# Kernel tuning notes

Measured on AMD Instinct MI355X. Metric: run time of the kernel, lower is better.

The kernel has to match this reference:

```python
import jax, jax.numpy as jnp
import numpy as np

D_MODEL = 1024
H = 16
D_K = D_MODEL // H
B = 2
S = 2048


def setup_inputs() -> dict:
    key = jax.random.key(0)
    ks = jax.random.split(key, 13)
    scale = 1.0 / np.sqrt(D_MODEL)
    inp = {
        "Q": jax.random.normal(ks[0], (B, S, D_MODEL), jnp.float32),
        "K": jax.random.normal(ks[1], (B, S, D_MODEL), jnp.float32),
        "V": jax.random.normal(ks[2], (B, S, D_MODEL), jnp.float32),
        "mask": jax.random.randint(ks[3], (B, 1, S, S), 0, 2, jnp.int32),
        "WQ_w": jax.random.normal(ks[4], (D_MODEL, D_MODEL), jnp.float32) * scale,
        "WQ_b": jax.random.normal(ks[5], (D_MODEL,), jnp.float32) * scale,
        "WK_w": jax.random.normal(ks[6], (D_MODEL, D_MODEL), jnp.float32) * scale,
        "WK_b": jax.random.normal(ks[7], (D_MODEL,), jnp.float32) * scale,
        "WV_w": jax.random.normal(ks[8], (D_MODEL, D_MODEL), jnp.float32) * scale,
        "WV_b": jax.random.normal(ks[9], (D_MODEL,), jnp.float32) * scale,
        "WO_w": jax.random.normal(ks[10], (D_MODEL, D_MODEL), jnp.float32) * scale,
        "WO_b": jax.random.normal(ks[11], (D_MODEL,), jnp.float32) * scale,
    }
    return inp


def _split_heads(x):
    # [B,S,D] -> [B,H,S,d_k]
    b, s, _ = x.shape
    return x.reshape(b, s, H, D_K).transpose(0, 2, 1, 3)


def reference(Q, K, V, mask, WQ_w, WQ_b, WK_w, WK_b, WV_w, WV_b, WO_w, WO_b):
    q = _split_heads(Q @ WQ_w.T + WQ_b)
    k = _split_heads(K @ WK_w.T + WK_b)
    v = _split_heads(V @ WV_w.T + WV_b)
    scores = jnp.einsum("bhqd,bhkd->bhqk", q, k) / jnp.sqrt(jnp.float32(D_K))
    # NOTE: original code fills masked positions with 1e-9 (not -inf) -- replicate faithfully
    scores = jnp.where(mask == 0, jnp.float32(1e-9), scores)
    attn = jax.nn.softmax(scores, axis=-1)
    out = jnp.einsum("bhqk,bhkd->bhqd", attn, v)  # [B,H,S,d_k]
    out = out.transpose(0, 2, 1, 3).reshape(Q.shape[0], -1, D_MODEL)
    return out @ WO_w.T + WO_b
```

## Files before the change

### kernel.cpp

```cpp
#include <hip/hip_runtime.h>
#include <stdint.h>

#define D_MODEL 1024
#define NH 16
#define DKK 64
#define SEQ 2048
#define QSCALE 0.18033688011112042f

using half8 = __attribute__((ext_vector_type(8))) _Float16;
using half4 = __attribute__((ext_vector_type(4))) _Float16;
using half2v = __attribute__((ext_vector_type(2))) _Float16;
using fp16x2 = __attribute__((ext_vector_type(2))) __fp16;
using f32x4 = __attribute__((ext_vector_type(4))) float;
using f32x16 = __attribute__((ext_vector_type(16))) float;

__device__ __forceinline__ f32x4 fz4() { f32x4 v = {0.f, 0.f, 0.f, 0.f}; return v; }

__device__ __forceinline__ void gload16(const void* g, void* l) {
    __builtin_amdgcn_global_load_lds(
        (const __attribute__((address_space(1))) unsigned int*)g,
        (__attribute__((address_space(3))) unsigned int*)l, 16, 0, 0);
}

__device__ __forceinline__ half2v pk2(float a, float b) {
    fp16x2 t = __builtin_amdgcn_cvt_pkrtz(a, b);
    return __builtin_bit_cast(half2v, t);
}

__device__ __forceinline__ half4 pk4(float a, float b, float c, float d) {
    half2v lo = pk2(a, b);
    half2v hi = pk2(c, d);
    half4 r; r.x = lo.x; r.y = lo.y; r.z = hi.x; r.w = hi.y;
    return r;
}

__device__ __forceinline__ int xswz(int bid, int n) {
    return (bid & 7) * (n >> 3) + (bid >> 3);
}

__global__ __launch_bounds__(256) void conv_all(const float* __restrict__ wq,
                                                const float* __restrict__ wk,
                                                const float* __restrict__ wv,
                                                const float* __restrict__ wo,
                                                const float* __restrict__ Q,
                                                const float* __restrict__ K,
                                                const float* __restrict__ V,
                                                _Float16* __restrict__ out) {
    int idx = blockIdx.x * 256 + threadIdx.x;
#pragma unroll
    for (int k = 0; k < 8; ++k) {
        int c = idx + k * 524288;
        const float* src;
        int off;
        if (c < 1048576) {
            int w = c >> 18;
            src = (w == 0) ? wq : (w == 1) ? wk : (w == 2) ? wv : wo;
            off = c & 0x3ffff;
        } else {
            int j = (c >> 20) - 1;
            src = (j == 0) ? Q : (j == 1) ? K : V;
            off = c & 0xfffff;
        }
        float4 v = ((const float4*)src)[off];
        ((half4*)out)[c] = pk4(v.x, v.y, v.z, v.w);
    }
}

__global__ __launch_bounds__(256) void pack_mask_k(const int* __restrict__ mask,
                                                   unsigned int* __restrict__ mbits) {
    int wid = threadIdx.x >> 6, lane = threadIdx.x & 63;
    int row = blockIdx.x * 4 + wid;
    const int* mrow = mask + (size_t)row * SEQ;
    unsigned int* orow = mbits + (size_t)row * (SEQ / 32);
    for (int it = 0; it < SEQ / 64; ++it) {
        int v = mrow[it * 64 + lane];
        unsigned long long bal = __ballot(v != 0);
        if (lane == 0)       orow[it * 2]     = (unsigned int)(bal & 0xffffffffull);
        else if (lane == 32) orow[it * 2 + 1] = (unsigned int)(bal >> 32);
    }
}

__device__ __forceinline__ void gemm_body(const _Float16* __restrict__ A,
                                          const _Float16* __restrict__ Wh,
                                          const float* __restrict__ bias,
                                          void* __restrict__ outp, int omode, float scale) {
    __shared__ __align__(16) _Float16 Asm[2][64 * 64];
    __shared__ __align__(16) _Float16 Bsm[2][128 * 64];
    const int tid = threadIdx.x;
    const int wg = xswz(blockIdx.x, 512);
    const int bm = wg >> 3, bn = wg & 7;
    const int wid = tid >> 6, lane = tid & 63;
    const int li = lane & 15, g = lane >> 4;
    const int wm = wid >> 1, wn = wid & 1;

    const int brow = wid * 32 + (lane >> 3);
    const char* bsrc = (const char*)(Wh + (size_t)(bn * 128 + brow) * D_MODEL)
                       + (((lane & 7) ^ (brow & 7)) * 16);
    const int bdst = wid * 32 * 128;
    const int arow = wid * 16 + (lane >> 3);
    const char* asrc = (const char*)(A + (size_t)(bm * 64 + arow) * D_MODEL)
                       + (((lane & 7) ^ (arow & 7)) * 16);
    const int adst = wid * 16 * 128;

    f32x4 acc[2][4];
#pragma unroll
    for (int i = 0; i < 2; ++i)
#pragma unroll
        for (int j = 0; j < 4; ++j) acc[i][j] = fz4();

    const int o0 = ((g << 4))      ^ ((li & 7) << 4);
    const int o1 = (64 + (g << 4)) ^ ((li & 7) << 4);
    const int abase = wm * 4096 + li * 128;
    const int bbase = wn * 8192 + li * 128;

    auto stage = [&](int it, int buf) {
        const char* bs = bsrc + it * 128;
        char* bd = (char*)&Bsm[buf][0] + bdst;
        gload16(bs,             bd);
        gload16(bs +  8 * 2048, bd + 1024);
        gload16(bs + 16 * 2048, bd + 2048);
        gload16(bs + 24 * 2048, bd + 3072);
        const char* as = asrc + it * 128;
        char* ad = (char*)&Asm[buf][0] + adst;
        gload16(as,            ad);
        gload16(as + 8 * 2048, ad + 1024);
    };

    stage(0, 0);
    __syncthreads();

    for (int it = 0; it < 16; ++it) {
        const int cur = it & 1;
        if (it + 1 < 16) stage(it + 1, cur ^ 1);
        const char* ab = (const char*)&Asm[cur][0];
        const char* bb = (const char*)&Bsm[cur][0];
#pragma unroll
        for (int s = 0; s < 2; ++s) {
            const int oS = s ? o1 : o0;
            half8 af0 = *(const half8*)(ab + abase + 0    + oS);
            half8 af1 = *(const half8*)(ab + abase + 2048 + oS);
            half8 bf[4];
#pragma unroll
            for (int nt = 0; nt < 4; ++nt)
                bf[nt] = *(const half8*)(bb + bbase + nt * 2048 + oS);
#pragma unroll
            for (int nt = 0; nt < 4; ++nt) {
                acc[0][nt] = __builtin_amdgcn_mfma_f32_16x16x32_f16(af0, bf[nt], acc[0][nt], 0, 0, 0);
                acc[1][nt] = __builtin_amdgcn_mfma_f32_16x16x32_f16(af1, bf[nt], acc[1][nt], 0, 0, 0);
            }
        }
        __syncthreads();
    }

#pragma unroll
    for (int nt = 0; nt < 4; ++nt) {
        int n = bn * 128 + wn * 64 + nt * 16 + li;
        float bv = bias[n];
#pragma unroll
        for (int mt = 0; mt < 2; ++mt) {
            if (omode == 1) {
                int s0 = bm * 64 + wm * 32 + mt * 16 + g * 4;
                int b = (bm * 64) >> 11;
                int h = n >> 6, d = n & 63;
                half4 hv = pk4(acc[mt][nt][0] + bv, acc[mt][nt][1] + bv,
                               acc[mt][nt][2] + bv, acc[mt][nt][3] + bv);
                *(half4*)((_Float16*)outp +
                          ((((size_t)(b * NH + h)) * DKK + d) * SEQ + (s0 & (SEQ - 1)))) = hv;
            } else {
#pragma unroll
                for (int r = 0; r < 4; ++r) {
                    int m = bm * 64 + wm * 32 + mt * 16 + g * 4 + r;
                    float val = (acc[mt][nt][r] + bv) * scale;
                    if (omode == 2) {
                        ((float*)outp)[(size_t)m * D_MODEL + n] = val;
                    } else {
                        int b = m >> 11, s = m & (SEQ - 1);
                        int h = n >> 6, d = n & 63;
                        ((_Float16*)outp)[(((size_t)(b * NH + h)) * SEQ + s) * DKK + d] =
                            (_Float16)val;
                    }
                }
            }
        }
    }
}

struct QkvArgs {
    const float *b0, *b1, *b2;
    _Float16 *o0, *o1, *o2;
};

__global__ __launch_bounds__(256) void gemm_qkv(const _Float16* __restrict__ Ah,
                                                const _Float16* __restrict__ cw,
                                                QkvArgs ga) {
    const int z = blockIdx.y;
    const _Float16* A  = Ah + (size_t)z * (D_MODEL * 4096);
    const float* bi = (z == 0) ? ga.b0 : (z == 1) ? ga.b1 : ga.b2;
    _Float16*    o  = (z == 0) ? ga.o0 : (z == 1) ? ga.o1 : ga.o2;
    gemm_body(A, cw + (size_t)z * D_MODEL * D_MODEL, bi, o,
              (z == 2) ? 1 : 0, (z == 0) ? QSCALE : 1.0f);
}

__global__ __launch_bounds__(256) void gemm_out(const _Float16* __restrict__ A,
                                                const _Float16* __restrict__ cw,
                                                const float* __restrict__ bias,
                                                float* __restrict__ out) {
    gemm_body(A, cw, bias, out, 2, 1.0f);
}

__global__ __launch_bounds__(256, 4) void attn_fwd(const _Float16* __restrict__ q,
                                                   const _Float16* __restrict__ kk,
                                                   const _Float16* __restrict__ vt,
                                                   const unsigned int* __restrict__ mb,
                                                   _Float16* __restrict__ aout) {
    __shared__ __align__(16) char smem[32768];
    const int wg = xswz(blockIdx.x, 1024);
    const int qblk = wg & 31, bh = wg >> 5;
    const int b = bh >> 4, h = bh & 15;
    const int tid = threadIdx.x, wid = tid >> 6, lane = tid & 63;
    const int l31 = lane & 31, hi = lane >> 5;
    const int qh = wid & 1, kh = wid >> 1;
    const _Float16* qp = q  + (size_t)bh * SEQ * DKK;
    const _Float16* kp = kk + (size_t)bh * SEQ * DKK;
    const _Float16* vp = vt + (size_t)bh * DKK * SEQ;
    const int qrow = qblk * 64 + qh * 32 + l31;

    half8 qf[4];
#pragma unroll
    for (int s = 0; s < 4; ++s)
        qf[s] = *(const half8*)(qp + (size_t)qrow * DKK + s * 16 + hi * 8);

    const int srow = wid * 16 + (lane >> 3);
    const int sswz = ((lane & 7) ^ (srow & 7)) * 16;
    const char* ksrc = (const char*)(kp + (size_t)srow * DKK) + sswz;
    const char* vsrc = (const char*)(vp + (size_t)srow * SEQ) + sswz;
    const int sdst = wid * 2048;

    auto stage = [&](int it, int buf) {
        const char* ks = ksrc + (size_t)it * 8192;
        const char* vs = vsrc + (size_t)it * 128;
        char* kd = smem + buf * 8192 + sdst;
        char* vd = smem + 16384 + buf * 8192 + sdst;
        gload16(ks,                       kd);
        gload16(ks + 8 * 128,             kd + 1024);
        gload16(vs,                       vd);
        gload16(vs + 8 * (size_t)SEQ * 2, vd + 1024);
    };

    f32x16 O0, O1;
#pragma unroll
    for (int j = 0; j < 16; ++j) { O0[j] = 0.f; O1[j] = 0.f; }
    float lsum = 0.f;

    const unsigned int* mrow = mb + (size_t)(b * SEQ + qrow) * (SEQ / 32);

    const int krow = kh * 32 + l31;
    const int kbase = krow * 128;
    const int krx = (krow & 7);
    const int v0row = l31;
    const int v1row = 32 + l31;

    stage(0, 0);
    __syncthreads();

    for (int it = 0; it < SEQ / 64; ++it) {
        const int cur = it & 1;
        if (it + 1 < SEQ / 64) stage(it + 1, cur ^ 1);
        const unsigned mw = mrow[it * 2 + kh] >> (hi * 4);

        f32x16 st;
#pragma unroll
        for (int j = 0; j < 16; ++j) st[j] = 0.f;
        const char* kb_ = smem + cur * 8192;
        __builtin_amdgcn_s_setprio(1);
#pragma unroll
        for (int s = 0; s < 4; ++s) {
            const int c = s * 2 + hi;
            half8 kf = *(const half8*)(kb_ + kbase + ((c ^ krx) << 4));
            st = __builtin_amdgcn_mfma_f32_32x32x16_f16(kf, qf[s], st, 0, 0, 0);
        }
        __builtin_amdgcn_s_setprio(0);

        unsigned w[8];
#pragma unroll
        for (int rq = 0; rq < 4; ++rq) {
            float e0 = __builtin_amdgcn_exp2f(st[rq * 4 + 0]);
            float e1 = __builtin_amdgcn_exp2f(st[rq * 4 + 1]);
            float e2 = __builtin_amdgcn_exp2f(st[rq * 4 + 2]);
            float e3 = __builtin_amdgcn_exp2f(st[rq * 4 + 3]);
            float p0 = ((mw >> (8 * rq + 0)) & 1u) ? e0 : 1.0f;
            float p1 = ((mw >> (8 * rq + 1)) & 1u) ? e1 : 1.0f;
            float p2 = ((mw >> (8 * rq + 2)) & 1u) ? e2 : 1.0f;
            float p3 = ((mw >> (8 * rq + 3)) & 1u) ? e3 : 1.0f;
            lsum += (p0 + p1) + (p2 + p3);
            w[2 * rq]     = __builtin_bit_cast(unsigned, pk2(p0, p1));
            w[2 * rq + 1] = __builtin_bit_cast(unsigned, pk2(p2, p3));
        }

        half8 pfrag[2];
#pragma unroll
        for (int s2 = 0; s2 < 2; ++s2) {
            unsigned a0 = w[s2 * 4 + 0], a1 = w[s2 * 4 + 1];
            unsigned a2 = w[s2 * 4 + 2], a3 = w[s2 * 4 + 3];
            unsigned t0 = (unsigned)__shfl_xor((int)(hi ? a0 : a2), 32);
            unsigned t1 = (unsigned)__shfl_xor((int)(hi ? a1 : a3), 32);
            uint4 f;
            f.x = hi ? t0 : a0;
            f.y = hi ? t1 : a1;
            f.z = hi ? a2 : t0;
            f.w = hi ? a3 : t1;
            pfrag[s2] = __builtin_bit_cast(half8, f);
        }

        const char* vb_ = smem + 16384 + cur * 8192;
        __builtin_amdgcn_s_setprio(1);
#pragma unroll
        for (int s2 = 0; s2 < 2; ++s2) {
            const int c = kh * 4 + s2 * 2 + hi;
            half8 vf0 = *(const half8*)(vb_ + v0row * 128 + ((c ^ (v0row & 7)) << 4));
            half8 vf1 = *(const half8*)(vb_ + v1row * 128 + ((c ^ (v1row & 7)) << 4));
            O0 = __builtin_amdgcn_mfma_f32_32x32x16_f16(vf0, pfrag[s2], O0, 0, 0, 0);
            O1 = __builtin_amdgcn_mfma_f32_32x32x16_f16(vf1, pfrag[s2], O1, 0, 0, 0);
        }
        __builtin_amdgcn_s_setprio(0);
        __syncthreads();
    }

    lsum += __shfl_xor(lsum, 32);

    const int SSTR = 36;
    float* scr = (float*)smem;
    float* lscr = (float*)(smem + 2 * 64 * SSTR * 4);
    if (kh == 1) {
        float* dst = scr + (size_t)qh * (64 * SSTR) + lane * SSTR;
#pragma unroll
        for (int j = 0; j < 4; ++j) {
            *(f32x4*)(dst + j * 4)      = *((f32x4*)&O0 + j);
            *(f32x4*)(dst + 16 + j * 4) = *((f32x4*)&O1 + j);
        }
        if (hi == 0) lscr[qh * 32 + l31] = lsum;
    }
    __syncthreads();
    if (kh == 0) {
        const float* src = scr + (size_t)qh * (64 * SSTR) + lane * SSTR;
#pragma unroll
        for (int j = 0; j < 16; ++j) { O0[j] += src[j]; O1[j] += src[16 + j]; }
        float inv = 1.0f / (lsum + lscr[qh * 32 + l31]);
        _Float16* orow = aout + ((size_t)(b * SEQ + qrow)) * D_MODEL + h * DKK + hi * 4;
#pragma unroll
        for (int rq = 0; rq < 4; ++rq) {
            *(half4*)(orow + 8 * rq) =
                pk4(O0[rq * 4 + 0] * inv, O0[rq * 4 + 1] * inv,
                    O0[rq * 4 + 2] * inv, O0[rq * 4 + 3] * inv);
            *(half4*)(orow + 32 + 8 * rq) =
                pk4(O1[rq * 4 + 0] * inv, O1[rq * 4 + 1] * inv,
                    O1[rq * 4 + 2] * inv, O1[rq * 4 + 3] * inv);
        }
    }
}

extern "C" void kernel_launch(void* const* d_in, const int* in_sizes, int n_in,
                              void* d_out, int out_size, void* d_ws, size_t ws_size,
                              hipStream_t stream) {
    const float* Q    = (const float*)d_in[0];
    const float* Kin  = (const float*)d_in[1];
    const float* Vin  = (const float*)d_in[2];
    const int*   mask = (const int*)d_in[3];
    const float* WQw = (const float*)d_in[4];
    const float* WQb = (const float*)d_in[5];
    const float* WKw = (const float*)d_in[6];
    const float* WKb = (const float*)d_in[7];
    const float* WVw = (const float*)d_in[8];
    const float* WVb = (const float*)d_in[9];
    const float* WOw = (const float*)d_in[10];
    const float* WOb = (const float*)d_in[11];

    char* w = (char*)d_ws;
    const size_t MB = 1ull << 20;
    _Float16* cw  = (_Float16*)(w);
    _Float16* Ah  = (_Float16*)(w + 8 * MB);
    _Float16* ab  = (_Float16*)(w + 8 * MB);
    _Float16* qb  = (_Float16*)(w + 32 * MB);
    _Float16* kbf = (_Float16*)(w + 40 * MB);
    _Float16* vtb = (_Float16*)(w + 48 * MB);
    unsigned int* mbits = (unsigned int*)(w + 56 * MB);

    conv_all<<<dim3(2048), dim3(256), 0, stream>>>(WQw, WKw, WVw, WOw, Q, Kin, Vin, cw);
    pack_mask_k<<<dim3(1024), dim3(256), 0, stream>>>(mask, mbits);

    QkvArgs ga;
    ga.b0 = WQb; ga.b1 = WKb; ga.b2 = WVb;
    ga.o0 = qb;  ga.o1 = kbf; ga.o2 = vtb;
    gemm_qkv<<<dim3(512, 3), dim3(256), 0, stream>>>(Ah, cw, ga);

    attn_fwd<<<dim3(1024), dim3(256), 0, stream>>>(qb, kbf, vtb, mbits, ab);

    gemm_out<<<dim3(512), dim3(256), 0, stream>>>(ab, cw + 3ull * D_MODEL * D_MODEL, WOb,
                                                  (float*)d_out);
}
```

Baseline: 146.5 us.

## Split attention KV range in two workgroups and combine partials in separate kernel

Each attention workgroup now processes half of the key/value sequence, doubling the grid to 2048 workgroups, and writes unnormalized fp16 partial outputs plus row sums to workspace. A new combine kernel adds the two halves, divides by the summed denominators and writes the head-interleaved layout. The row sum is now computed with an extra MFMA against a ones vector instead of scalar adds, and the occupancy hint rises to 5 workgroups per SIMD. The goal is better load balance and occupancy across the compute units, paid for with an extra launch, more global traffic for the partials, and fp16 rounding of the unnormalized partial sums.

```diff
diff --git a/kernel.cpp b/kernel.cpp
--- a/kernel.cpp
+++ b/kernel.cpp
@@ -208,15 +208,16 @@
     gemm_body(A, cw, bias, out, 2, 1.0f);
 }
 
-__global__ __launch_bounds__(256, 4) void attn_fwd(const _Float16* __restrict__ q,
+__global__ __launch_bounds__(256, 5) void attn_fwd(const _Float16* __restrict__ q,
                                                    const _Float16* __restrict__ kk,
                                                    const _Float16* __restrict__ vt,
                                                    const unsigned int* __restrict__ mb,
-                                                   _Float16* __restrict__ aout) {
+                                                   _Float16* __restrict__ opart,
+                                                   float* __restrict__ lpart) {
     __shared__ __align__(16) char smem[32768];
-    const int wg = xswz(blockIdx.x, 1024);
-    const int qblk = wg & 31, bh = wg >> 5;
-    const int b = bh >> 4, h = bh & 15;
+    const int wg = xswz(blockIdx.x, 2048);
+    const int qblk = wg & 31, kvh = (wg >> 5) & 1, bh = wg >> 6;
+    const int b = bh >> 4;
     const int tid = threadIdx.x, wid = tid >> 6, lane = tid & 63;
     const int l31 = lane & 31, hi = lane >> 5;
     const int qh = wid & 1, kh = wid >> 1;
@@ -229,6 +230,10 @@
 #pragma unroll
     for (int s = 0; s < 4; ++s)
         qf[s] = *(const half8*)(qp + (size_t)qrow * DKK + s * 16 + hi * 8);
+
+    half8 ones;
+#pragma unroll
+    for (int j = 0; j < 8; ++j) ones[j] = (_Float16)1.0f;
 
     const int srow = wid * 16 + (lane >> 3);
     const int sswz = ((lane & 7) ^ (srow & 7)) * 16;
@@ -247,10 +252,9 @@
         gload16(vs + 8 * (size_t)SEQ * 2, vd + 1024);
     };
 
-    f32x16 O0, O1;
-#pragma unroll
-    for (int j = 0; j < 16; ++j) { O0[j] = 0.f; O1[j] = 0.f; }
-    float lsum = 0.f;
+    f32x16 O0, O1, Ol;
+#pragma unroll
+    for (int j = 0; j < 16; ++j) { O0[j] = 0.f; O1[j] = 0.f; Ol[j] = 0.f; }
 
     const unsigned int* mrow = mb + (size_t)(b * SEQ + qrow) * (SEQ / 32);
 
@@ -260,12 +264,14 @@
     const int v0row = l31;
     const int v1row = 32 + l31;
 
-    stage(0, 0);
+    const int it0 = kvh * 16;
+    stage(it0, 0);
     __syncthreads();
 
-    for (int it = 0; it < SEQ / 64; ++it) {
-        const int cur = it & 1;
-        if (it + 1 < SEQ / 64) stage(it + 1, cur ^ 1);
+    for (int t = 0; t < 16; ++t) {
+        const int it = it0 + t;
+        const int cur = t & 1;
+        if (t + 1 < 16) stage(it + 1, cur ^ 1);
         const unsigned mw = mrow[it * 2 + kh] >> (hi * 4);
 
         f32x16 st;
@@ -292,7 +298,6 @@
             float p1 = ((mw >> (8 * rq + 1)) & 1u) ? e1 : 1.0f;
             float p2 = ((mw >> (8 * rq + 2)) & 1u) ? e2 : 1.0f;
             float p3 = ((mw >> (8 * rq + 3)) & 1u) ? e3 : 1.0f;
-            lsum += (p0 + p1) + (p2 + p3);
             w[2 * rq]     = __builtin_bit_cast(unsigned, pk2(p0, p1));
             w[2 * rq + 1] = __builtin_bit_cast(unsigned, pk2(p2, p3));
         }
@@ -319,6 +324,7 @@
             const int c = kh * 4 + s2 * 2 + hi;
             half8 vf0 = *(const half8*)(vb_ + v0row * 128 + ((c ^ (v0row & 7)) << 4));
             half8 vf1 = *(const half8*)(vb_ + v1row * 128 + ((c ^ (v1row & 7)) << 4));
+            Ol = __builtin_amdgcn_mfma_f32_32x32x16_f16(ones, pfrag[s2], Ol, 0, 0, 0);
             O0 = __builtin_amdgcn_mfma_f32_32x32x16_f16(vf0, pfrag[s2], O0, 0, 0, 0);
             O1 = __builtin_amdgcn_mfma_f32_32x32x16_f16(vf1, pfrag[s2], O1, 0, 0, 0);
         }
@@ -326,7 +332,7 @@
         __syncthreads();
     }
 
-    lsum += __shfl_xor(lsum, 32);
+    float lsum = Ol[0];
 
     const int SSTR = 36;
     float* scr = (float*)smem;
@@ -345,18 +351,36 @@
         const float* src = scr + (size_t)qh * (64 * SSTR) + lane * SSTR;
 #pragma unroll
         for (int j = 0; j < 16; ++j) { O0[j] += src[j]; O1[j] += src[16 + j]; }
-        float inv = 1.0f / (lsum + lscr[qh * 32 + l31]);
-        _Float16* orow = aout + ((size_t)(b * SEQ + qrow)) * D_MODEL + h * DKK + hi * 4;
+        lsum += lscr[qh * 32 + l31];
+        const size_t row = (size_t)bh * SEQ + qrow;
+        _Float16* od = opart + (size_t)kvh * (65536ull * 64) + row * 64 + hi * 4;
 #pragma unroll
         for (int rq = 0; rq < 4; ++rq) {
-            *(half4*)(orow + 8 * rq) =
-                pk4(O0[rq * 4 + 0] * inv, O0[rq * 4 + 1] * inv,
-                    O0[rq * 4 + 2] * inv, O0[rq * 4 + 3] * inv);
-            *(half4*)(orow + 32 + 8 * rq) =
-                pk4(O1[rq * 4 + 0] * inv, O1[rq * 4 + 1] * inv,
-                    O1[rq * 4 + 2] * inv, O1[rq * 4 + 3] * inv);
-        }
-    }
+            *(half4*)(od + 8 * rq) =
+                pk4(O0[rq * 4 + 0], O0[rq * 4 + 1], O0[rq * 4 + 2], O0[rq * 4 + 3]);
+            *(half4*)(od + 32 + 8 * rq) =
+                pk4(O1[rq * 4 + 0], O1[rq * 4 + 1], O1[rq * 4 + 2], O1[rq * 4 + 3]);
+        }
+        if (hi == 0) lpart[(size_t)kvh * 65536 + row] = lsum;
+    }
+}
+
+__global__ __launch_bounds__(256) void attn_combine(const _Float16* __restrict__ opart,
+                                                    const float* __restrict__ lpart,
+                                                    _Float16* __restrict__ ab) {
+    int gid = blockIdx.x * 256 + threadIdx.x;
+    int row = gid >> 3, q8 = gid & 7;
+    const half8 o0 = *(const half8*)(opart + (size_t)row * 64 + q8 * 8);
+    const half8 o1 = *(const half8*)(opart + 65536ull * 64 + (size_t)row * 64 + q8 * 8);
+    float inv = 1.0f / (lpart[row] + lpart[65536 + row]);
+    int bh = row >> 11, s = row & (SEQ - 1);
+    int b = bh >> 4, h = bh & 15;
+    _Float16* dst = ab + ((size_t)(b * SEQ + s)) * D_MODEL + h * DKK + q8 * 8;
+    half8 r;
+#pragma unroll
+    for (int j = 0; j < 8; ++j)
+        r[j] = (_Float16)(((float)o0[j] + (float)o1[j]) * inv);
+    *(half8*)dst = r;
 }
 
 extern "C" void kernel_launch(void* const* d_in, const int* in_sizes, int n_in,
@@ -377,13 +401,15 @@
 
     char* w = (char*)d_ws;
     const size_t MB = 1ull << 20;
-    _Float16* cw  = (_Float16*)(w);
-    _Float16* Ah  = (_Float16*)(w + 8 * MB);
-    _Float16* ab  = (_Float16*)(w + 8 * MB);
-    _Float16* qb  = (_Float16*)(w + 32 * MB);
-    _Float16* kbf = (_Float16*)(w + 40 * MB);
-    _Float16* vtb = (_Float16*)(w + 48 * MB);
+    _Float16* cw    = (_Float16*)(w);
+    _Float16* Ah    = (_Float16*)(w + 8 * MB);
+    _Float16* ab    = (_Float16*)(w + 8 * MB);
+    _Float16* opart = (_Float16*)(w + 16 * MB);
+    _Float16* qb    = (_Float16*)(w + 32 * MB);
+    _Float16* kbf   = (_Float16*)(w + 40 * MB);
+    _Float16* vtb   = (_Float16*)(w + 48 * MB);
     unsigned int* mbits = (unsigned int*)(w + 56 * MB);
+    float* lpart    = (float*)(w + 57 * MB);
 
     conv_all<<<dim3(2048), dim3(256), 0, stream>>>(WQw, WKw, WVw, WOw, Q, Kin, Vin, cw);
     pack_mask_k<<<dim3(1024), dim3(256), 0, stream>>>(mask, mbits);
@@ -393,7 +419,8 @@
     ga.o0 = qb;  ga.o1 = kbf; ga.o2 = vtb;
     gemm_qkv<<<dim3(512, 3), dim3(256), 0, stream>>>(Ah, cw, ga);
 
-    attn_fwd<<<dim3(1024), dim3(256), 0, stream>>>(qb, kbf, vtb, mbits, ab);
+    attn_fwd<<<dim3(2048), dim3(256), 0, stream>>>(qb, kbf, vtb, mbits, opart, lpart);
+    attn_combine<<<dim3(2048), dim3(256), 0, stream>>>(opart, lpart, ab);
 
     gemm_out<<<dim3(512), dim3(256), 0, stream>>>(ab, cw + 3ull * D_MODEL * D_MODEL, WOb,
                                                   (float*)d_out);
```

Result: slower. 200.0 us (+36.5%).

## Make attention K staging per-wave, load V into registers, and merge prep kernels

Applied to the files above, without the earlier changes.

The prep kernels for fp16 conversion and mask packing are merged into one launch with a block-index split, saving one kernel launch. In attention, each wave now stages its own private K slice into LDS with a two-tile lookahead. V fragments are loaded straight from global memory into registers, double-buffered across tiles. This removes the per-iteration __syncthreads and V's LDS round trip, relying on explicit vmcnt waits instead. The cost is more VGPR pressure, redundant K loads across waves sharing the same rows, and uncoalesced per-lane V loads.

```diff
diff --git a/kernel.cpp b/kernel.cpp
--- a/kernel.cpp
+++ b/kernel.cpp
@@ -38,45 +38,47 @@
     return (bid & 7) * (n >> 3) + (bid >> 3);
 }
 
-__global__ __launch_bounds__(256) void conv_all(const float* __restrict__ wq,
-                                                const float* __restrict__ wk,
-                                                const float* __restrict__ wv,
-                                                const float* __restrict__ wo,
-                                                const float* __restrict__ Q,
-                                                const float* __restrict__ K,
-                                                const float* __restrict__ V,
-                                                _Float16* __restrict__ out) {
-    int idx = blockIdx.x * 256 + threadIdx.x;
-#pragma unroll
-    for (int k = 0; k < 8; ++k) {
-        int c = idx + k * 524288;
-        const float* src;
-        int off;
-        if (c < 1048576) {
-            int w = c >> 18;
-            src = (w == 0) ? wq : (w == 1) ? wk : (w == 2) ? wv : wo;
-            off = c & 0x3ffff;
-        } else {
-            int j = (c >> 20) - 1;
-            src = (j == 0) ? Q : (j == 1) ? K : V;
-            off = c & 0xfffff;
-        }
-        float4 v = ((const float4*)src)[off];
-        ((half4*)out)[c] = pk4(v.x, v.y, v.z, v.w);
-    }
-}
-
-__global__ __launch_bounds__(256) void pack_mask_k(const int* __restrict__ mask,
-                                                   unsigned int* __restrict__ mbits) {
-    int wid = threadIdx.x >> 6, lane = threadIdx.x & 63;
-    int row = blockIdx.x * 4 + wid;
-    const int* mrow = mask + (size_t)row * SEQ;
-    unsigned int* orow = mbits + (size_t)row * (SEQ / 32);
-    for (int it = 0; it < SEQ / 64; ++it) {
-        int v = mrow[it * 64 + lane];
-        unsigned long long bal = __ballot(v != 0);
-        if (lane == 0)       orow[it * 2]     = (unsigned int)(bal & 0xffffffffull);
-        else if (lane == 32) orow[it * 2 + 1] = (unsigned int)(bal >> 32);
+__global__ __launch_bounds__(256) void prep(const float* __restrict__ wq,
+                                            const float* __restrict__ wk,
+                                            const float* __restrict__ wv,
+                                            const float* __restrict__ wo,
+                                            const float* __restrict__ Q,
+                                            const float* __restrict__ K,
+                                            const float* __restrict__ V,
+                                            const int* __restrict__ mask,
+                                            _Float16* __restrict__ out,
+                                            unsigned int* __restrict__ mbits) {
+    const int bid = blockIdx.x;
+    if (bid < 2048) {
+        int idx = bid * 256 + threadIdx.x;
+#pragma unroll
+        for (int k = 0; k < 8; ++k) {
+            int c = idx + k * 524288;
+            const float* src;
+            int off;
+            if (c < 1048576) {
+                int w = c >> 18;
+                src = (w == 0) ? wq : (w == 1) ? wk : (w == 2) ? wv : wo;
+                off = c & 0x3ffff;
+            } else {
+                int j = (c >> 20) - 1;
+                src = (j == 0) ? Q : (j == 1) ? K : V;
+                off = c & 0xfffff;
+            }
+            float4 v = ((const float4*)src)[off];
+            ((half4*)out)[c] = pk4(v.x, v.y, v.z, v.w);
+        }
+    } else {
+        int wid = threadIdx.x >> 6, lane = threadIdx.x & 63;
+        int row = (bid - 2048) * 4 + wid;
+        const int* mrow = mask + (size_t)row * SEQ;
+        unsigned int* orow = mbits + (size_t)row * (SEQ / 32);
+        for (int it = 0; it < SEQ / 64; ++it) {
+            int v = mrow[it * 64 + lane];
+            unsigned long long bal = __ballot(v != 0);
+            if (lane == 0)       orow[it * 2]     = (unsigned int)(bal & 0xffffffffull);
+            else if (lane == 32) orow[it * 2 + 1] = (unsigned int)(bal >> 32);
+        }
     }
 }
 
@@ -230,21 +232,28 @@
     for (int s = 0; s < 4; ++s)
         qf[s] = *(const half8*)(qp + (size_t)qrow * DKK + s * 16 + hi * 8);
 
-    const int srow = wid * 16 + (lane >> 3);
-    const int sswz = ((lane & 7) ^ (srow & 7)) * 16;
-    const char* ksrc = (const char*)(kp + (size_t)srow * DKK) + sswz;
-    const char* vsrc = (const char*)(vp + (size_t)srow * SEQ) + sswz;
-    const int sdst = wid * 2048;
-
-    auto stage = [&](int it, int buf) {
+    const int srow = kh * 32 + (lane >> 3);
+    const char* ksrc = (const char*)(kp + (size_t)srow * DKK)
+                       + (((lane & 7) ^ (srow & 7)) * 16);
+    const int kregion = wid * 4096;
+    auto stageK = [&](int it, int buf) {
         const char* ks = ksrc + (size_t)it * 8192;
-        const char* vs = vsrc + (size_t)it * 128;
-        char* kd = smem + buf * 8192 + sdst;
-        char* vd = smem + 16384 + buf * 8192 + sdst;
-        gload16(ks,                       kd);
-        gload16(ks + 8 * 128,             kd + 1024);
-        gload16(vs,                       vd);
-        gload16(vs + 8 * (size_t)SEQ * 2, vd + 1024);
+        char* kd = smem + buf * 16384 + kregion;
+        gload16(ks,            kd);
+        gload16(ks +  8 * 128, kd + 1024);
+        gload16(ks + 16 * 128, kd + 2048);
+        gload16(ks + 24 * 128, kd + 3072);
+    };
+
+    const _Float16* vbase = vp + (size_t)l31 * SEQ + kh * 32 + hi * 8;
+    half8 vA[4], vB[4];
+    auto loadV = [&](int it, half8 (&vr)[4]) {
+        const _Float16* vb = vbase + it * 64;
+#pragma unroll
+        for (int d0 = 0; d0 < 2; ++d0)
+#pragma unroll
+            for (int s2 = 0; s2 < 2; ++s2)
+                vr[d0 * 2 + s2] = *(const half8*)(vb + (size_t)d0 * 32 * SEQ + s2 * 16);
     };
 
     f32x16 O0, O1;
@@ -253,30 +262,27 @@
     float lsum = 0.f;
 
     const unsigned int* mrow = mb + (size_t)(b * SEQ + qrow) * (SEQ / 32);
-
-    const int krow = kh * 32 + l31;
-    const int kbase = krow * 128;
-    const int krx = (krow & 7);
-    const int v0row = l31;
-    const int v1row = 32 + l31;
-
-    stage(0, 0);
-    __syncthreads();
-
-    for (int it = 0; it < SEQ / 64; ++it) {
-        const int cur = it & 1;
-        if (it + 1 < SEQ / 64) stage(it + 1, cur ^ 1);
+    const int kbase = kregion + l31 * 128;
+    const int krx = (l31 & 7);
+
+    stageK(0, 0); loadV(0, vA);
+    stageK(1, 1); loadV(1, vB);
+
+    auto tile = [&](int it, int cur, half8 (&vr)[4]) {
         const unsigned mw = mrow[it * 2 + kh] >> (hi * 4);
 
+        asm volatile("s_waitcnt vmcnt(12)" ::: "memory");
+        __builtin_amdgcn_sched_barrier(0);
+
         f32x16 st;
 #pragma unroll
         for (int j = 0; j < 16; ++j) st[j] = 0.f;
-        const char* kb_ = smem + cur * 8192;
+        const char* kb_ = smem + cur * 16384 + kbase;
         __builtin_amdgcn_s_setprio(1);
 #pragma unroll
         for (int s = 0; s < 4; ++s) {
             const int c = s * 2 + hi;
-            half8 kf = *(const half8*)(kb_ + kbase + ((c ^ krx) << 4));
+            half8 kf = *(const half8*)(kb_ + ((c ^ krx) << 4));
             st = __builtin_amdgcn_mfma_f32_32x32x16_f16(kf, qf[s], st, 0, 0, 0);
         }
         __builtin_amdgcn_s_setprio(0);
@@ -312,20 +318,23 @@
             pfrag[s2] = __builtin_bit_cast(half8, f);
         }
 
-        const char* vb_ = smem + 16384 + cur * 8192;
         __builtin_amdgcn_s_setprio(1);
 #pragma unroll
         for (int s2 = 0; s2 < 2; ++s2) {
-            const int c = kh * 4 + s2 * 2 + hi;
-            half8 vf0 = *(const half8*)(vb_ + v0row * 128 + ((c ^ (v0row & 7)) << 4));
-            half8 vf1 = *(const half8*)(vb_ + v1row * 128 + ((c ^ (v1row & 7)) << 4));
-            O0 = __builtin_amdgcn_mfma_f32_32x32x16_f16(vf0, pfrag[s2], O0, 0, 0, 0);
-            O1 = __builtin_amdgcn_mfma_f32_32x32x16_f16(vf1, pfrag[s2], O1, 0, 0, 0);
+            O0 = __builtin_amdgcn_mfma_f32_32x32x16_f16(vr[s2],     pfrag[s2], O0, 0, 0, 0);
+            O1 = __builtin_amdgcn_mfma_f32_32x32x16_f16(vr[2 + s2], pfrag[s2], O1, 0, 0, 0);
         }
         __builtin_amdgcn_s_setprio(0);
-        __syncthreads();
-    }
-
+
+        if (it + 2 < SEQ / 64) { stageK(it + 2, cur); loadV(it + 2, vr); }
+    };
+
+    for (int i2 = 0; i2 < SEQ / 128; ++i2) {
+        tile(2 * i2,     0, vA);
+        tile(2 * i2 + 1, 1, vB);
+    }
+
+    __syncthreads();
     lsum += __shfl_xor(lsum, 32);
 
     const int SSTR = 36;
@@ -385,8 +394,8 @@
     _Float16* vtb = (_Float16*)(w + 48 * MB);
     unsigned int* mbits = (unsigned int*)(w + 56 * MB);
 
-    conv_all<<<dim3(2048), dim3(256), 0, stream>>>(WQw, WKw, WVw, WOw, Q, Kin, Vin, cw);
-    pack_mask_k<<<dim3(1024), dim3(256), 0, stream>>>(mask, mbits);
+    prep<<<dim3(3072), dim3(256), 0, stream>>>(WQw, WKw, WVw, WOw, Q, Kin, Vin, mask,
+                                               cw, mbits);
 
     QkvArgs ga;
     ga.b0 = WQb; ga.b1 = WKb; ga.b2 = WVb;
```

Measured after the change: 174.5 us. +19.1%, slower.
